# Performance work log

Hardware: AMD Instinct MI355X
Metric: run time of the kernel (lower is better)

## Reference

```python
import jax, jax.numpy as jnp
import numpy as np

N = 50000      # nodes
E = 800000     # edges (avg degree 16)
LM = 768       # lm_input_dim
H = 192        # hidden_dim = 32*6
B6 = 32        # per-branch dim = hidden_dim/6
SLOPE = 0.01   # nn.LeakyReLU default negative slope


def setup_inputs() -> dict:
    key = jax.random.key(0)
    ks = jax.random.split(key, 32)
    f = lambda i, shape, s=0.05: (jax.random.normal(ks[i], shape, jnp.float32) * s)
    inp = {
        "pre_x": f(0, (N, LM)),
        "x": f(1, (N, LM)),
        "edge_index": jax.random.randint(ks[2], (2, E), 0, N),
        "edge_type": jax.random.randint(ks[3], (E,), 0, 3),
        "num_prop": f(4, (N, 5)),
        "num_category": f(5, (N, 1)),
        "des_tensor": f(6, (N, LM)),
        "tweet_tensor": f(7, (N, LM)),
        # parameters (torch nn.Linear convention: W is [out, in], y = x @ W.T + b)
        "W_des": f(8, (B6, LM)), "b_des": f(9, (B6,)),
        "W_tweet": f(10, (B6, LM)), "b_tweet": f(11, (B6,)),
        "W_tweet_tr": f(12, (B6, LM)), "b_tweet_tr": f(13, (B6,)),
        "W_prop": f(14, (B6, 5)), "b_prop": f(15, (B6,)),
        "W_cat": f(16, (B6, 1)), "b_cat": f(17, (B6,)),
        "W_text": f(18, (B6, LM)), "b_text": f(19, (B6,)),
        "W_in": f(20, (H, H)), "b_in": f(21, (H,)),
        "W_c1": f(22, (H, H)), "b_c1": f(23, (H,)),
        "W_c2": f(24, (H, H)), "b_c2": f(25, (H,)),
        "W_o1": f(26, (96, H)), "b_o1": f(27, (96,)),
        "W_o2": f(28, (2, 96)), "b_o2": f(29, (2,)),
    }
    return inp


def _gcn_conv(h, W, b, src, dst):
    """PyG GCNConv: symmetric-normalized aggregation with added self-loops.
    out[v] = sum_{u->v} (d_u d_v)^{-1/2} (h_u W^T) + (1/d_v) (h_v W^T) + b
    where d includes the self-loop (+1)."""
    n = h.shape[0]
    hW = h @ W.T                                                  # [N, H]
    deg = jax.ops.segment_sum(jnp.ones(src.shape[0], h.dtype), dst,
                              num_segments=n) + 1.0               # [N]
    dinv = jax.lax.rsqrt(deg)
    norm = dinv[src] * dinv[dst]                                  # [E]
    agg = jax.ops.segment_sum(hW[src] * norm[:, None], dst,
                              num_segments=n)                     # [N, H]
    return agg + hW * (1.0 / deg)[:, None] + b


def reference(pre_x, x, edge_index, edge_type, num_prop, num_category,
              des_tensor, tweet_tensor,
              W_des, b_des, W_tweet, b_tweet, W_tweet_tr, b_tweet_tr,
              W_prop, b_prop, W_cat, b_cat, W_text, b_text,
              W_in, b_in, W_c1, b_c1, W_c2, b_c2,
              W_o1, b_o1, W_o2, b_o2):
    lrelu = lambda v: jax.nn.leaky_relu(v, SLOPE)
    branch = lambda t, W, b: lrelu(t @ W.T + b)   # dropout is identity in eval

    d = branch(des_tensor, W_des, b_des)
    pre_t = branch(pre_x, W_tweet, b_tweet)
    t = branch(x, W_tweet_tr, b_tweet_tr)
    n = branch(num_prop, W_prop, b_prop)
    c = branch(num_category, W_cat, b_cat)
    tw = branch(tweet_tensor, W_text, b_text)

    h = jnp.concatenate((n, c, d, tw, pre_t, t), axis=1)          # [N, 192]
    h = lrelu(h @ W_in.T + b_in)

    src, dst = edge_index[0], edge_index[1]
    h = _gcn_conv(h, W_c1, b_c1, src, dst)
    h = _gcn_conv(h, W_c2, b_c2, src, dst)

    em = lrelu(h @ W_o1.T + b_o1)                                 # [N, 96]
    out = em @ W_o2.T + b_o2                                      # [N, 2]
    return (out, em)
```

## Files before the change

### kernel.cpp

```cpp
#include <hip/hip_runtime.h>

#define NN 50000
#define EE 800000
#define LMD 768
#define HD 192
#define SLOPE 0.01f

typedef short bf16x8 __attribute__((ext_vector_type(8)));
typedef float f32x4 __attribute__((ext_vector_type(4)));
typedef unsigned short u16;

__device__ __forceinline__ float lrelu(float v){ return v > 0.f ? v : SLOPE * v; }

__device__ __forceinline__ u16 f2bf(float f){
    unsigned u = __float_as_uint(f);
    u += 0x7FFF + ((u >> 16) & 1u);
    return (u16)(u >> 16);
}
__device__ __forceinline__ float bf2f(u16 v){
    return __uint_as_float(((unsigned)v) << 16);
}
__device__ __forceinline__ bf16x8 as_bf8(float4 v){
    union { float4 f; bf16x8 b; } u; u.f = v; return u.b;
}

__global__ __launch_bounds__(256) void k_prep(
    const float* __restrict__ W0, const float* __restrict__ W1,
    const float* __restrict__ W2, const float* __restrict__ W3,
    const float* __restrict__ Win, const float* __restrict__ Wc1,
    const float* __restrict__ Wc2, const float* __restrict__ Wo1,
    u16* __restrict__ out)
{
    int m = blockIdx.y;
    int idx = blockIdx.x * 256 + threadIdx.x;
    const float* src; int nelem; int K;
    switch (m) {
      case 0: src = W0;  nelem = 32*768;  K = 768; break;
      case 1: src = W1;  nelem = 32*768;  K = 768; break;
      case 2: src = W2;  nelem = 32*768;  K = 768; break;
      case 3: src = W3;  nelem = 32*768;  K = 768; break;
      case 4: src = Win; nelem = 192*192; K = 192; break;
      case 5: src = Wc1; nelem = 192*192; K = 192; break;
      case 6: src = Wc2; nelem = 192*192; K = 192; break;
      default: src = Wo1; nelem = 96*192; K = 192; break;
    }
    if (idx >= nelem) return;
    u16 v = f2bf(src[idx]);
    int c = idx / K, k = idx - c * K;
    int cb = c >> 4, lr = c & 15;
    int sg = k >> 5, kk = k & 31, hi = kk >> 3, j = kk & 7;
    int lane = hi * 16 + lr;
    size_t dst;
    if (m < 4)      dst = (size_t)m * 24576 + (sg * 2 + cb) * 512 + lane * 8 + j;
    else if (m < 7) dst = 98304 + (size_t)(m - 4) * 36864 + (sg * 12 + cb) * 512 + lane * 8 + j;
    else            dst = 208896 + (size_t)(sg * 6 + cb) * 512 + lane * 8 + j;
    out[dst] = v;
}

__global__ __launch_bounds__(256, 4) void k_branch(
    const float* __restrict__ des, const float* __restrict__ twt,
    const float* __restrict__ prex, const float* __restrict__ xx,
    const u16* __restrict__ Wf,
    const float* __restrict__ bd, const float* __restrict__ btx,
    const float* __restrict__ btw, const float* __restrict__ btr,
    const float* __restrict__ nprop, const float* __restrict__ ncat,
    const float* __restrict__ Wp, const float* __restrict__ bp,
    const float* __restrict__ Wc, const float* __restrict__ bc,
    u16* __restrict__ h)
{
    __shared__ u16 Abuf[16][776];
    __shared__ float scr[4][16][32];

    const int br = blockIdx.y;
    const float* A; const float* bias; int colBase;
    switch (br) {
      case 0:  A = des;  bias = bd;  colBase = 64;  break;
      case 1:  A = twt;  bias = btx; colBase = 96;  break;
      case 2:  A = prex; bias = btw; colBase = 128; break;
      default: A = xx;   bias = btr; colBase = 160; break;
    }

    const int t0 = threadIdx.x, w = t0 >> 6, l = t0 & 63;
    const int hi = l >> 4, lr = l & 15;

    bf16x8 Bfr[12];
    {
        const u16* wp = Wf + br * 24576;
        #pragma unroll
        for (int cc = 0; cc < 6; ++cc)
            #pragma unroll
            for (int cb = 0; cb < 2; ++cb)
                Bfr[cc * 2 + cb] = *(const bf16x8*)(wp + ((w * 6 + cc) * 2 + cb) * 512 + l * 8);
    }

    const int rrow = t0 >> 4;
    const int col0 = (t0 & 15) * 2;
    const float bias0 = bias[col0], bias1 = bias[col0 + 1];

    float4 f4[12];
    int tile = blockIdx.x;
    {
        const float* ab = A + (size_t)tile * 12288 + w * 3072 + l * 4;
        #pragma unroll
        for (int i = 0; i < 12; ++i) f4[i] = *(const float4*)(ab + i * 256);
    }

    for (; tile < 3125; tile += 256) {
        asm volatile("s_waitcnt vmcnt(0)" ::: "memory");
        #pragma unroll
        for (int i = 0; i < 12; ++i) {
            const int rr = i / 3, third = i % 3;
            uint2 pk;
            pk.x = (unsigned)f2bf(f4[i].x) | ((unsigned)f2bf(f4[i].y) << 16);
            pk.y = (unsigned)f2bf(f4[i].z) | ((unsigned)f2bf(f4[i].w) << 16);
            *(uint2*)&Abuf[w * 4 + rr][third * 256 + l * 4] = pk;
        }
        const int tnext = tile + 256;
        if (tnext < 3125) {
            const float* ab = A + (size_t)tnext * 12288 + w * 3072 + l * 4;
            #pragma unroll
            for (int i = 0; i < 12; ++i) f4[i] = *(const float4*)(ab + i * 256);
        }
        __syncthreads();

        f32x4 acc[2] = {};
        #pragma unroll
        for (int cc = 0; cc < 6; ++cc) {
            const int cg = w * 6 + cc;
            bf16x8 af = *(const bf16x8*)&Abuf[lr][cg * 32 + hi * 8];
            acc[0] = __builtin_amdgcn_mfma_f32_16x16x32_bf16(af, Bfr[cc * 2 + 0], acc[0], 0, 0, 0);
            acc[1] = __builtin_amdgcn_mfma_f32_16x16x32_bf16(af, Bfr[cc * 2 + 1], acc[1], 0, 0, 0);
        }
        #pragma unroll
        for (int cb = 0; cb < 2; ++cb)
            #pragma unroll
            for (int rg = 0; rg < 4; ++rg)
                scr[w][hi * 4 + rg][cb * 16 + lr] = acc[cb][rg];
        __syncthreads();

        float2 s; s.x = 0.f; s.y = 0.f;
        #pragma unroll
        for (int ww = 0; ww < 4; ++ww) {
            float2 p = *(const float2*)&scr[ww][rrow][col0];
            s.x += p.x; s.y += p.y;
        }
        unsigned pk = (unsigned)f2bf(lrelu(s.x + bias0)) | ((unsigned)f2bf(lrelu(s.y + bias1)) << 16);
        *(unsigned*)&h[((size_t)tile * 16 + rrow) * HD + colBase + col0] = pk;

        if (br == 0) {
            const int c0 = (t0 & 15) * 4;
            const size_t row = (size_t)tile * 16 + rrow;
            float o[4];
            #pragma unroll
            for (int j = 0; j < 4; ++j) {
                int c = c0 + j;
                float accv;
                if (c < 32) {
                    accv = bp[c];
                    #pragma unroll
                    for (int k = 0; k < 5; ++k) accv += nprop[row * 5 + k] * Wp[c * 5 + k];
                } else {
                    accv = bc[c - 32] + ncat[row] * Wc[c - 32];
                }
                o[j] = lrelu(accv);
            }
            uint2 pk2;
            pk2.x = (unsigned)f2bf(o[0]) | ((unsigned)f2bf(o[1]) << 16);
            pk2.y = (unsigned)f2bf(o[2]) | ((unsigned)f2bf(o[3]) << 16);
            *(uint2*)&h[row * HD + c0] = pk2;
        }
    }
}

__global__ __launch_bounds__(512) void k_hgemm2(
    const u16* __restrict__ A, const u16* __restrict__ Wf1, const u16* __restrict__ Wf2,
    const float* __restrict__ b1, u16* __restrict__ out)
{
    __shared__ u16 h1s[128 * 192];
    const int t = threadIdx.x, w = t >> 6, l = t & 63;
    const int hi = l >> 4, lr = l & 15;
    const int rowBase = blockIdx.x * 128;
    int r0 = rowBase + w * 16 + lr;
    int rowc = r0 < NN ? r0 : NN - 1;
    const u16* ap = A + (size_t)rowc * HD;

    bf16x8 afr[6];
    #pragma unroll
    for (int sg = 0; sg < 6; ++sg)
        afr[sg] = *(const bf16x8*)(ap + sg * 32 + hi * 8);

    f32x4 acc[12] = {};
    #pragma unroll
    for (int sg = 0; sg < 6; ++sg)
        #pragma unroll
        for (int cb = 0; cb < 12; ++cb) {
            bf16x8 bf = *(const bf16x8*)(Wf1 + (sg * 12 + cb) * 512 + l * 8);
            acc[cb] = __builtin_amdgcn_mfma_f32_16x16x32_bf16(afr[sg], bf, acc[cb], 0, 0, 0);
        }

    #pragma unroll
    for (int cb = 0; cb < 12; ++cb) {
        int cl = cb * 16 + lr;
        float bv = b1[cl];
        #pragma unroll
        for (int rg = 0; rg < 4; ++rg) {
            int rr = w * 16 + hi * 4 + rg;
            int colp = (((cl >> 3) ^ (rr & 7)) << 3) | (cl & 7);
            h1s[rr * 192 + colp] = f2bf(lrelu(acc[cb][rg] + bv));
        }
    }
    __syncthreads();

    int rr2 = w * 16 + lr;
    bf16x8 af2[6];
    #pragma unroll
    for (int sg = 0; sg < 6; ++sg) {
        int chunk = (sg * 4 + hi) ^ (rr2 & 7);
        af2[sg] = *(const bf16x8*)&h1s[rr2 * 192 + chunk * 8];
    }

    f32x4 acc2[12] = {};
    #pragma unroll
    for (int sg = 0; sg < 6; ++sg)
        #pragma unroll
        for (int cb = 0; cb < 12; ++cb) {
            bf16x8 bf = *(const bf16x8*)(Wf2 + (sg * 12 + cb) * 512 + l * 8);
            acc2[cb] = __builtin_amdgcn_mfma_f32_16x16x32_bf16(af2[sg], bf, acc2[cb], 0, 0, 0);
        }

    #pragma unroll
    for (int cb = 0; cb < 12; ++cb) {
        int cl = cb * 16 + lr;
        #pragma unroll
        for (int rg = 0; rg < 4; ++rg) {
            int r = rowBase + w * 16 + hi * 4 + rg;
            if (r < NN) out[(size_t)r * HD + cl] = f2bf(acc2[cb][rg]);
        }
    }
}

template<bool BIAS, bool LRELU>
__global__ __launch_bounds__(512) void k_hgemm(
    const u16* __restrict__ A, const u16* __restrict__ Wf,
    const float* __restrict__ bias, u16* __restrict__ out)
{
    __shared__ u16 Bs[36864];
    const int t = threadIdx.x, w = t >> 6, l = t & 63;
    const int hi = l >> 4, lr = l & 15;
    const int rowBase = blockIdx.x * 128;
    {
        const uint4* s_ = (const uint4*)Wf; uint4* d_ = (uint4*)Bs;
        #pragma unroll
        for (int i = 0; i < 9; ++i) d_[i * 512 + t] = s_[i * 512 + t];
    }
    int r0 = rowBase + w * 16 + lr;
    int rowc = r0 < NN ? r0 : NN - 1;
    const u16* ap = A + (size_t)rowc * HD;
    float4 araw[6];
    #pragma unroll
    for (int sg = 0; sg < 6; ++sg) {
        araw[sg] = *(const float4*)(ap + sg * 32 + hi * 8);
        asm volatile("" :: "v"(araw[sg].x), "v"(araw[sg].y), "v"(araw[sg].z), "v"(araw[sg].w));
    }
    __syncthreads();

    f32x4 acc[12] = {};
    #pragma unroll
    for (int sg = 0; sg < 6; ++sg) {
        bf16x8 af = as_bf8(araw[sg]);
        #pragma unroll
        for (int cb = 0; cb < 12; ++cb) {
            bf16x8 bf = *(const bf16x8*)(Bs + (sg * 12 + cb) * 512 + l * 8);
            acc[cb] = __builtin_amdgcn_mfma_f32_16x16x32_bf16(af, bf, acc[cb], 0, 0, 0);
        }
    }

    #pragma unroll
    for (int cb = 0; cb < 12; ++cb) {
        int cl = cb * 16 + lr;
        float bv = BIAS ? bias[cl] : 0.f;
        #pragma unroll
        for (int rg = 0; rg < 4; ++rg) {
            int r = rowBase + w * 16 + hi * 4 + rg;
            if (r < NN) {
                float v = acc[cb][rg] + bv;
                if (LRELU) v = lrelu(v);
                out[(size_t)r * HD + cl] = f2bf(v);
            }
        }
    }
}

__global__ __launch_bounds__(512) void k_final(
    const u16* __restrict__ A, const u16* __restrict__ Wf,
    const float* __restrict__ b1, const float* __restrict__ W2,
    const float* __restrict__ b2, float* __restrict__ em, float* __restrict__ out)
{
    __shared__ u16 Bs[18432];
    const int t = threadIdx.x, w = t >> 6, l = t & 63;
    const int hi = l >> 4, lr = l & 15;
    const int rowBase = blockIdx.x * 128;
    {
        const uint4* s_ = (const uint4*)Wf; uint4* d_ = (uint4*)Bs;
        #pragma unroll
        for (int i = 0; i < 5; ++i) { int idx = i * 512 + t; if (idx < 2304) d_[idx] = s_[idx]; }
    }
    int r0 = rowBase + w * 16 + lr;
    int rowc = r0 < NN ? r0 : NN - 1;
    const u16* ap = A + (size_t)rowc * HD;
    float4 araw[6];
    #pragma unroll
    for (int sg = 0; sg < 6; ++sg) {
        araw[sg] = *(const float4*)(ap + sg * 32 + hi * 8);
        asm volatile("" :: "v"(araw[sg].x), "v"(araw[sg].y), "v"(araw[sg].z), "v"(araw[sg].w));
    }
    __syncthreads();

    f32x4 acc[6] = {};
    #pragma unroll
    for (int sg = 0; sg < 6; ++sg) {
        bf16x8 af = as_bf8(araw[sg]);
        #pragma unroll
        for (int cb = 0; cb < 6; ++cb) {
            bf16x8 bf = *(const bf16x8*)(Bs + (sg * 6 + cb) * 512 + l * 8);
            acc[cb] = __builtin_amdgcn_mfma_f32_16x16x32_bf16(af, bf, acc[cb], 0, 0, 0);
        }
    }

    float w2v[2][6], bv[6];
    #pragma unroll
    for (int cb = 0; cb < 6; ++cb) {
        bv[cb] = b1[cb * 16 + lr];
        w2v[0][cb] = W2[cb * 16 + lr];
        w2v[1][cb] = W2[96 + cb * 16 + lr];
    }

    #pragma unroll
    for (int rg = 0; rg < 4; ++rg) {
        int r = rowBase + w * 16 + hi * 4 + rg;
        float o0 = 0.f, o1 = 0.f;
        #pragma unroll
        for (int cb = 0; cb < 6; ++cb) {
            float v = lrelu(acc[cb][rg] + bv[cb]);
            if (r < NN) em[(size_t)r * 96 + cb * 16 + lr] = v;
            o0 += v * w2v[0][cb];
            o1 += v * w2v[1][cb];
        }
        #pragma unroll
        for (int d = 1; d < 16; d <<= 1) {
            o0 += __shfl_xor(o0, d);
            o1 += __shfl_xor(o1, d);
        }
        if (lr == 0 && r < NN) {
            out[r * 2 + 0] = o0 + b2[0];
            out[r * 2 + 1] = o1 + b2[1];
        }
    }
}

__global__ void k_count(const int* __restrict__ ei, int* __restrict__ deg)
{
    int e = blockIdx.x * 256 + threadIdx.x;
    if (e < EE) atomicAdd(&deg[ei[EE + e]], 1);
}

__global__ __launch_bounds__(1024) void k_scan1(const int* __restrict__ deg, int* __restrict__ rp,
                                                int* __restrict__ part,
                                                float* __restrict__ dinv, float* __restrict__ invdeg)
{
    __shared__ int sh[1024];
    int tid = threadIdx.x, i = blockIdx.x * 1024 + tid;
    int x = (i < NN) ? deg[i] : 0;
    if (i < NN) {
        float d = (float)(x + 1);
        dinv[i] = rsqrtf(d);
        invdeg[i] = 1.0f / d;
    }
    sh[tid] = x;
    __syncthreads();
    for (int off = 1; off < 1024; off <<= 1) {
        int y = (tid >= off) ? sh[tid - off] : 0;
        __syncthreads();
        sh[tid] += y;
        __syncthreads();
    }
    if (i < NN) rp[i] = sh[tid] - x;
    if (tid == 1023) part[blockIdx.x] = sh[tid];
}

__global__ void k_scan2(int* part, int nb, int* rp)
{
    if (threadIdx.x == 0 && blockIdx.x == 0) {
        int run = 0;
        for (int b = 0; b < nb; ++b) { int t = part[b]; part[b] = run; run += t; }
        rp[NN] = run;
    }
}

__global__ void k_scan3(int* rp, const int* __restrict__ part, int* __restrict__ cursor)
{
    int i = blockIdx.x * 256 + threadIdx.x;
    if (i < NN) {
        int v = rp[i] + part[i >> 10];
        rp[i] = v;
        cursor[i] = v;
    }
}

__global__ void k_fill(const int* __restrict__ ei, const float* __restrict__ dinv,
                       int* __restrict__ cursor, int* __restrict__ cs, float* __restrict__ nrm)
{
    int e = blockIdx.x * 256 + threadIdx.x;
    if (e >= EE) return;
    int s = ei[e], d = ei[EE + e];
    int pos = atomicAdd(&cursor[d], 1);
    cs[pos] = s;
    nrm[pos] = dinv[s] * dinv[d];
}

__global__ __launch_bounds__(240) void k_agg(const u16* __restrict__ hW,
    const int* __restrict__ rp, const int* __restrict__ cs, const float* __restrict__ nrm,
    const float* __restrict__ invdeg, const float* __restrict__ bias, u16* __restrict__ out)
{
    int v = blockIdx.x * 5 + threadIdx.y;
    int f0 = threadIdx.x * 4;
    int s0 = rp[v], s1 = rp[v + 1];
    float4 bv = *reinterpret_cast<const float4*>(bias + f0);
    ushort4 hv = *reinterpret_cast<const ushort4*>(hW + (size_t)v * HD + f0);
    float idg = invdeg[v];
    float a0 = bf2f(hv.x) * idg + bv.x;
    float a1 = bf2f(hv.y) * idg + bv.y;
    float a2 = bf2f(hv.z) * idg + bv.z;
    float a3 = bf2f(hv.w) * idg + bv.w;
    int i = s0;
    for (; i + 4 <= s1; i += 4) {
        int c0 = cs[i], c1 = cs[i+1], c2 = cs[i+2], c3 = cs[i+3];
        float n0 = nrm[i], n1 = nrm[i+1], n2 = nrm[i+2], n3 = nrm[i+3];
        ushort4 g0 = *reinterpret_cast<const ushort4*>(hW + (size_t)c0 * HD + f0);
        ushort4 g1 = *reinterpret_cast<const ushort4*>(hW + (size_t)c1 * HD + f0);
        ushort4 g2 = *reinterpret_cast<const ushort4*>(hW + (size_t)c2 * HD + f0);
        ushort4 g3 = *reinterpret_cast<const ushort4*>(hW + (size_t)c3 * HD + f0);
        a0 += bf2f(g0.x) * n0; a1 += bf2f(g0.y) * n0; a2 += bf2f(g0.z) * n0; a3 += bf2f(g0.w) * n0;
        a0 += bf2f(g1.x) * n1; a1 += bf2f(g1.y) * n1; a2 += bf2f(g1.z) * n1; a3 += bf2f(g1.w) * n1;
        a0 += bf2f(g2.x) * n2; a1 += bf2f(g2.y) * n2; a2 += bf2f(g2.z) * n2; a3 += bf2f(g2.w) * n2;
        a0 += bf2f(g3.x) * n3; a1 += bf2f(g3.y) * n3; a2 += bf2f(g3.z) * n3; a3 += bf2f(g3.w) * n3;
    }
    for (; i < s1; ++i) {
        int c = cs[i]; float n = nrm[i];
        ushort4 g = *reinterpret_cast<const ushort4*>(hW + (size_t)c * HD + f0);
        a0 += bf2f(g.x) * n; a1 += bf2f(g.y) * n; a2 += bf2f(g.z) * n; a3 += bf2f(g.w) * n;
    }
    ushort4 o;
    o.x = f2bf(a0); o.y = f2bf(a1); o.z = f2bf(a2); o.w = f2bf(a3);
    *reinterpret_cast<ushort4*>(out + (size_t)v * HD + f0) = o;
}

extern "C" void kernel_launch(void* const* d_in, const int* in_sizes, int n_in,
                              void* d_out, int out_size, void* d_ws, size_t ws_size,
                              hipStream_t stream)
{
    const float* pre_x = (const float*)d_in[0];
    const float* x     = (const float*)d_in[1];
    const int*   ei    = (const int*)d_in[2];
    const float* nprop = (const float*)d_in[4];
    const float* ncat  = (const float*)d_in[5];
    const float* des   = (const float*)d_in[6];
    const float* twt   = (const float*)d_in[7];
    const float* W_des  = (const float*)d_in[8],  *b_des  = (const float*)d_in[9];
    const float* W_tw   = (const float*)d_in[10], *b_tw   = (const float*)d_in[11];
    const float* W_tr   = (const float*)d_in[12], *b_tr   = (const float*)d_in[13];
    const float* W_prop = (const float*)d_in[14], *b_prop = (const float*)d_in[15];
    const float* W_cat  = (const float*)d_in[16], *b_cat  = (const float*)d_in[17];
    const float* W_text = (const float*)d_in[18], *b_text = (const float*)d_in[19];
    const float* W_in   = (const float*)d_in[20], *b_in   = (const float*)d_in[21];
    const float* W_c1   = (const float*)d_in[22], *b_c1   = (const float*)d_in[23];
    const float* W_c2   = (const float*)d_in[24], *b_c2   = (const float*)d_in[25];
    const float* W_o1   = (const float*)d_in[26], *b_o1   = (const float*)d_in[27];
    const float* W_o2   = (const float*)d_in[28], *b_o2   = (const float*)d_in[29];

    char* base = (char*)d_ws;
    size_t off = 0;
    auto alloc = [&](size_t bytes) -> char* {
        char* p = base + off;
        off = (off + bytes + 255) & ~(size_t)255;
        return p;
    };
    u16*   hA     = (u16*)alloc((size_t)NN * HD * 2);
    u16*   hB     = (u16*)alloc((size_t)NN * HD * 2);
    u16*   hC     = (u16*)alloc((size_t)NN * HD * 2);
    u16*   Wprep  = (u16*)alloc((size_t)227328 * 2);
    float* dinv   = (float*)alloc((size_t)NN * 4);
    float* invdeg = (float*)alloc((size_t)NN * 4);
    int*   deg    = (int*)alloc((size_t)NN * 4);
    int*   rp     = (int*)alloc((size_t)(NN + 1) * 4);
    int*   cursor = (int*)alloc((size_t)NN * 4);
    int*   part   = (int*)alloc(64 * 4);
    int*   cs     = (int*)alloc((size_t)EE * 4);
    float* nrm    = (float*)alloc((size_t)EE * 4);
    (void)ws_size; (void)in_sizes; (void)n_in; (void)out_size;

    float* outp = (float*)d_out;
    float* em   = outp + (size_t)NN * 2;

    const int rb     = (NN + 255) / 256;
    const int rb128  = (NN + 127) / 128;
    const int eb     = (EE + 255) / 256;
    const int nb1024 = (NN + 1023) / 1024;

    hipMemsetAsync(deg, 0, (size_t)NN * 4, stream);
    hipLaunchKernelGGL(k_prep, dim3(144, 8), dim3(256), 0, stream,
        W_des, W_text, W_tw, W_tr, W_in, W_c1, W_c2, W_o1, Wprep);
    hipLaunchKernelGGL(k_count,  dim3(eb), dim3(256), 0, stream, ei, deg);
    hipLaunchKernelGGL(k_scan1,  dim3(nb1024), dim3(1024), 0, stream, deg, rp, part, dinv, invdeg);
    hipLaunchKernelGGL(k_scan2,  dim3(1), dim3(1), 0, stream, part, nb1024, rp);
    hipLaunchKernelGGL(k_scan3,  dim3(rb), dim3(256), 0, stream, rp, part, cursor);
    hipLaunchKernelGGL(k_fill,   dim3(eb), dim3(256), 0, stream, ei, dinv, cursor, cs, nrm);

    hipLaunchKernelGGL(k_branch, dim3(256, 4), dim3(256), 0, stream,
        des, twt, pre_x, x, Wprep, b_des, b_text, b_tw, b_tr,
        nprop, ncat, W_prop, b_prop, W_cat, b_cat, hA);

    hipLaunchKernelGGL(k_hgemm2, dim3(rb128), dim3(512), 0, stream,
        hA, Wprep + 98304, Wprep + 98304 + 36864, b_in, hB);
    hipLaunchKernelGGL(k_agg, dim3(NN / 5), dim3(48, 5), 0, stream, hB, rp, cs, nrm, invdeg, b_c1, hC);
    hipLaunchKernelGGL((k_hgemm<false, false>), dim3(rb128), dim3(512), 0, stream,
        hC, Wprep + 98304 + 2 * 36864, nullptr, hA);
    hipLaunchKernelGGL(k_agg, dim3(NN / 5), dim3(48, 5), 0, stream, hA, rp, cs, nrm, invdeg, b_c2, hB);

    hipLaunchKernelGGL(k_final, dim3(rb128), dim3(512), 0, stream,
        hB, Wprep + 208896, b_o1, W_o2, b_o2, em, outp);
}
```

Measured before the change: 460.3 us.

## Compute edge norms on the fly, split small branches, retune branch grid

The per-edge normalization array is no longer stored during CSR fill. The aggregation kernel now computes dinv[src]*dinv[dst] itself, which removes a 3.2MB write and its reads but adds a random gather of dinv per edge. The prop/category branch moves out of the branch GEMM kernel into its own elementwise kernel, taking the branch divergence off block row 0. The branch GEMM grid shrinks from 256 to 192 blocks per branch, and its occupancy hint drops to 3 waves.

```diff
diff --git a/kernel.cpp b/kernel.cpp
--- a/kernel.cpp
+++ b/kernel.cpp
@@ -57,15 +57,12 @@
     out[dst] = v;
 }
 
-__global__ __launch_bounds__(256, 4) void k_branch(
+__global__ __launch_bounds__(256, 3) void k_branch(
     const float* __restrict__ des, const float* __restrict__ twt,
     const float* __restrict__ prex, const float* __restrict__ xx,
     const u16* __restrict__ Wf,
     const float* __restrict__ bd, const float* __restrict__ btx,
     const float* __restrict__ btw, const float* __restrict__ btr,
-    const float* __restrict__ nprop, const float* __restrict__ ncat,
-    const float* __restrict__ Wp, const float* __restrict__ bp,
-    const float* __restrict__ Wc, const float* __restrict__ bc,
     u16* __restrict__ h)
 {
     __shared__ u16 Abuf[16][776];
@@ -105,7 +102,7 @@
         for (int i = 0; i < 12; ++i) f4[i] = *(const float4*)(ab + i * 256);
     }
 
-    for (; tile < 3125; tile += 256) {
+    for (; tile < 3125; tile += 192) {
         asm volatile("s_waitcnt vmcnt(0)" ::: "memory");
         #pragma unroll
         for (int i = 0; i < 12; ++i) {
@@ -115,7 +112,7 @@
             pk.y = (unsigned)f2bf(f4[i].z) | ((unsigned)f2bf(f4[i].w) << 16);
             *(uint2*)&Abuf[w * 4 + rr][third * 256 + l * 4] = pk;
         }
-        const int tnext = tile + 256;
+        const int tnext = tile + 192;
         if (tnext < 3125) {
             const float* ab = A + (size_t)tnext * 12288 + w * 3072 + l * 4;
             #pragma unroll
@@ -146,30 +143,28 @@
         }
         unsigned pk = (unsigned)f2bf(lrelu(s.x + bias0)) | ((unsigned)f2bf(lrelu(s.y + bias1)) << 16);
         *(unsigned*)&h[((size_t)tile * 16 + rrow) * HD + colBase + col0] = pk;
-
-        if (br == 0) {
-            const int c0 = (t0 & 15) * 4;
-            const size_t row = (size_t)tile * 16 + rrow;
-            float o[4];
-            #pragma unroll
-            for (int j = 0; j < 4; ++j) {
-                int c = c0 + j;
-                float accv;
-                if (c < 32) {
-                    accv = bp[c];
-                    #pragma unroll
-                    for (int k = 0; k < 5; ++k) accv += nprop[row * 5 + k] * Wp[c * 5 + k];
-                } else {
-                    accv = bc[c - 32] + ncat[row] * Wc[c - 32];
-                }
-                o[j] = lrelu(accv);
-            }
-            uint2 pk2;
-            pk2.x = (unsigned)f2bf(o[0]) | ((unsigned)f2bf(o[1]) << 16);
-            pk2.y = (unsigned)f2bf(o[2]) | ((unsigned)f2bf(o[3]) << 16);
-            *(uint2*)&h[row * HD + c0] = pk2;
-        }
-    }
+    }
+}
+
+__global__ __launch_bounds__(256) void k_small_branch(
+    const float* __restrict__ nprop, const float* __restrict__ ncat,
+    const float* __restrict__ Wp, const float* __restrict__ bp,
+    const float* __restrict__ Wc, const float* __restrict__ bc,
+    u16* __restrict__ h)
+{
+    int idx = blockIdx.x * 256 + threadIdx.x;
+    if (idx >= NN * 64) return;
+    int row = idx >> 6, c = idx & 63;
+    float acc;
+    if (c < 32) {
+        acc = bp[c];
+        #pragma unroll
+        for (int k = 0; k < 5; ++k) acc += nprop[row * 5 + k] * Wp[c * 5 + k];
+    } else {
+        int cc = c - 32;
+        acc = bc[cc] + ncat[row] * Wc[cc];
+    }
+    h[(size_t)row * HD + c] = f2bf(lrelu(acc));
 }
 
 __global__ __launch_bounds__(512) void k_hgemm2(
@@ -407,19 +402,18 @@
     }
 }
 
-__global__ void k_fill(const int* __restrict__ ei, const float* __restrict__ dinv,
-                       int* __restrict__ cursor, int* __restrict__ cs, float* __restrict__ nrm)
+__global__ void k_fill(const int* __restrict__ ei,
+                       int* __restrict__ cursor, int* __restrict__ cs)
 {
     int e = blockIdx.x * 256 + threadIdx.x;
     if (e >= EE) return;
     int s = ei[e], d = ei[EE + e];
     int pos = atomicAdd(&cursor[d], 1);
     cs[pos] = s;
-    nrm[pos] = dinv[s] * dinv[d];
 }
 
 __global__ __launch_bounds__(240) void k_agg(const u16* __restrict__ hW,
-    const int* __restrict__ rp, const int* __restrict__ cs, const float* __restrict__ nrm,
+    const int* __restrict__ rp, const int* __restrict__ cs, const float* __restrict__ dinv,
     const float* __restrict__ invdeg, const float* __restrict__ bias, u16* __restrict__ out)
 {
     int v = blockIdx.x * 5 + threadIdx.y;
@@ -428,6 +422,7 @@
     float4 bv = *reinterpret_cast<const float4*>(bias + f0);
     ushort4 hv = *reinterpret_cast<const ushort4*>(hW + (size_t)v * HD + f0);
     float idg = invdeg[v];
+    float dv = dinv[v];
     float a0 = bf2f(hv.x) * idg + bv.x;
     float a1 = bf2f(hv.y) * idg + bv.y;
     float a2 = bf2f(hv.z) * idg + bv.z;
@@ -435,7 +430,7 @@
     int i = s0;
     for (; i + 4 <= s1; i += 4) {
         int c0 = cs[i], c1 = cs[i+1], c2 = cs[i+2], c3 = cs[i+3];
-        float n0 = nrm[i], n1 = nrm[i+1], n2 = nrm[i+2], n3 = nrm[i+3];
+        float n0 = dinv[c0] * dv, n1 = dinv[c1] * dv, n2 = dinv[c2] * dv, n3 = dinv[c3] * dv;
         ushort4 g0 = *reinterpret_cast<const ushort4*>(hW + (size_t)c0 * HD + f0);
         ushort4 g1 = *reinterpret_cast<const ushort4*>(hW + (size_t)c1 * HD + f0);
         ushort4 g2 = *reinterpret_cast<const ushort4*>(hW + (size_t)c2 * HD + f0);
@@ -446,7 +441,7 @@
         a0 += bf2f(g3.x) * n3; a1 += bf2f(g3.y) * n3; a2 += bf2f(g3.z) * n3; a3 += bf2f(g3.w) * n3;
     }
     for (; i < s1; ++i) {
-        int c = cs[i]; float n = nrm[i];
+        int c = cs[i]; float n = dinv[c] * dv;
         ushort4 g = *reinterpret_cast<const ushort4*>(hW + (size_t)c * HD + f0);
         a0 += bf2f(g.x) * n; a1 += bf2f(g.y) * n; a2 += bf2f(g.z) * n; a3 += bf2f(g.w) * n;
     }
@@ -496,7 +491,6 @@
     int*   cursor = (int*)alloc((size_t)NN * 4);
     int*   part   = (int*)alloc(64 * 4);
     int*   cs     = (int*)alloc((size_t)EE * 4);
-    float* nrm    = (float*)alloc((size_t)EE * 4);
     (void)ws_size; (void)in_sizes; (void)n_in; (void)out_size;
 
     float* outp = (float*)d_out;
@@ -514,18 +508,19 @@
     hipLaunchKernelGGL(k_scan1,  dim3(nb1024), dim3(1024), 0, stream, deg, rp, part, dinv, invdeg);
     hipLaunchKernelGGL(k_scan2,  dim3(1), dim3(1), 0, stream, part, nb1024, rp);
     hipLaunchKernelGGL(k_scan3,  dim3(rb), dim3(256), 0, stream, rp, part, cursor);
-    hipLaunchKernelGGL(k_fill,   dim3(eb), dim3(256), 0, stream, ei, dinv, cursor, cs, nrm);
-
-    hipLaunchKernelGGL(k_branch, dim3(256, 4), dim3(256), 0, stream,
-        des, twt, pre_x, x, Wprep, b_des, b_text, b_tw, b_tr,
+    hipLaunchKernelGGL(k_fill,   dim3(eb), dim3(256), 0, stream, ei, cursor, cs);
+
+    hipLaunchKernelGGL(k_branch, dim3(192, 4), dim3(256), 0, stream,
+        des, twt, pre_x, x, Wprep, b_des, b_text, b_tw, b_tr, hA);
+    hipLaunchKernelGGL(k_small_branch, dim3((NN * 64 + 255) / 256), dim3(256), 0, stream,
         nprop, ncat, W_prop, b_prop, W_cat, b_cat, hA);
 
     hipLaunchKernelGGL(k_hgemm2, dim3(rb128), dim3(512), 0, stream,
         hA, Wprep + 98304, Wprep + 98304 + 36864, b_in, hB);
-    hipLaunchKernelGGL(k_agg, dim3(NN / 5), dim3(48, 5), 0, stream, hB, rp, cs, nrm, invdeg, b_c1, hC);
+    hipLaunchKernelGGL(k_agg, dim3(NN / 5), dim3(48, 5), 0, stream, hB, rp, cs, dinv, invdeg, b_c1, hC);
     hipLaunchKernelGGL((k_hgemm<false, false>), dim3(rb128), dim3(512), 0, stream,
         hC, Wprep + 98304 + 2 * 36864, nullptr, hA);
-    hipLaunchKernelGGL(k_agg, dim3(NN / 5), dim3(48, 5), 0, stream, hA, rp, cs, nrm, invdeg, b_c2, hB);
+    hipLaunchKernelGGL(k_agg, dim3(NN / 5), dim3(48, 5), 0, stream, hA, rp, cs, dinv, invdeg, b_c2, hB);
 
     hipLaunchKernelGGL(k_final, dim3(rb128), dim3(512), 0, stream,
         hB, Wprep + 208896, b_o1, W_o2, b_o2, em, outp);
```

Result: faster. 416.4 us (-9.6%).
